# Optimization experiments

Hardware: AMD Instinct MI355X
Metric: run time of the kernel (lower is better)

## Reference

```python
import jax, jax.numpy as jnp
import numpy as np

GAMMA = 1.0
BIG = 1e8  # boundary value used by the original numba kernel


def setup_inputs() -> dict:
    key = jax.random.key(0)
    k1, k2 = jax.random.split(key)
    N, M, d = 4096, 4096, 64
    x = jax.random.normal(k1, (N, d), dtype=jnp.float32)
    y = jax.random.normal(k2, (M, d), dtype=jnp.float32)
    return {"x": x, "y": y}


def _soft_dtw(D, gamma):
    """Soft-DTW DP R[N,M] via anti-diagonal wavefront scan.

    Matches compute_softdtw: R padded with BIG, R[0,0]=0,
    R[i,j] = D[i-1,j-1] + softmin_gamma(R[i-1,j-1], R[i-1,j], R[i,j-1]).
    Diagonals are stored as length-(N+2) vectors indexed by i (j = k - i).
    """
    N, M = D.shape
    ii = jnp.arange(1, N + 1)          # cell row indices 1..N
    inf = jnp.full((N + 2,), BIG, D.dtype)
    r_km2 = inf.at[0].set(0.0)          # diagonal k=0: only R[0,0]=0
    r_km1 = inf                         # diagonal k=1: all boundary

    def step(carry, k):
        r_km2, r_km1 = carry
        j = k - ii                      # column index per row on this diagonal
        valid = (j >= 1) & (j <= M)
        r0 = -r_km2[ii - 1] / gamma     # R[i-1, j-1]
        r1 = -r_km1[ii - 1] / gamma     # R[i-1, j]
        r2 = -r_km1[ii] / gamma         # R[i,   j-1]
        rmax = jnp.maximum(jnp.maximum(r0, r1), r2)
        rsum = jnp.exp(r0 - rmax) + jnp.exp(r1 - rmax) + jnp.exp(r2 - rmax)
        softmin = -gamma * (jnp.log(rsum) + rmax)
        jc = jnp.clip(j - 1, 0, M - 1)
        d_diag = D[ii - 1, jc]          # D[i-1, j-1] along this diagonal
        val = jnp.where(valid, d_diag + softmin, BIG)
        r_k = inf.at[1:N + 1].set(val)
        return (r_km1, r_k), None

    ks = jnp.arange(2, N + M + 1)
    (_, r_last), _ = jax.lax.scan(step, (r_km2, r_km1), ks)
    return r_last[N]                    # R[N, M]


def reference(x, y):
    # squared-euclidean distance matrix: sum((x_i - y_j)^2)
    x2 = jnp.sum(x * x, axis=1)
    y2 = jnp.sum(y * y, axis=1)
    D = x2[:, None] + y2[None, :] - 2.0 * (x @ y.T)  # [N, M]
    N, M = D.shape
    r = _soft_dtw(D, GAMMA)
    return r / (N + M)                   # open_end=False path
```

## Files before the change

### kernel.cpp

```cpp
#include <hip/hip_runtime.h>
#include <hip/hip_fp16.h>

#define Nn 4096
#define Mm 4096
#define NB 64
#define CH 16
#define NCHUNK 260
#define NCHUNKP 262
#define HPITCH 4352
#define HOFF 64
#define LOG2E 1.4426950408889634f
#define LN2 0.6931471805599453f
#define BIGX (1 << 23)

typedef unsigned long long ull;

__device__ __forceinline__ float hw_exp2(float x) { return __builtin_amdgcn_exp2f(x); }
__device__ __forceinline__ float hw_log2(float x) { return __builtin_amdgcn_logf(x); }

__device__ __forceinline__ float dpp_shr1(float v) {
    int r = __builtin_amdgcn_update_dpp(0, __float_as_int(v), 0x138, 0xF, 0xF, false);
    return __int_as_float(r);
}
__device__ __forceinline__ int dpp_shr1_i(int v) {
    return __builtin_amdgcn_update_dpp(0, v, 0x138, 0xF, 0xF, false);
}
__device__ __forceinline__ float dpp_shl1(float v) {
    int r = __builtin_amdgcn_update_dpp(0, __float_as_int(v), 0x130, 0xF, 0xF, false);
    return __int_as_float(r);
}
__device__ __forceinline__ int dpp_shl1_i(int v) {
    return __builtin_amdgcn_update_dpp(0, v, 0x130, 0xF, 0xF, false);
}
__device__ __forceinline__ float half_lo(int w) {
    return __low2float(__builtin_bit_cast(__half2, w));
}
__device__ __forceinline__ float half_hi(int w) {
    return __high2float(__builtin_bit_cast(__half2, w));
}
__device__ __forceinline__ ull packmx(float m, int X) {
    return (ull)__float_as_uint(m) | ((ull)(unsigned)X << 32);
}

__global__ __launch_bounds__(256) void dist_kernel(const float* __restrict__ x,
                                                   const float* __restrict__ y,
                                                   __half* __restrict__ Dsk) {
    __shared__ float xs[64][65];
    __shared__ float ys[80][65];
    __shared__ float dt[64][81];
    __shared__ float x2s[64], y2s[80];
    const int b = blockIdx.y, tj = blockIdx.x, tid = threadIdx.x;

    const float4* x4 = (const float4*)(x + (size_t)b * 64 * 64);
#pragma unroll
    for (int i = 0; i < 4; ++i) {
        int idx = tid + i * 256;
        int r = idx >> 4, c = (idx & 15) * 4;
        float4 v = x4[idx];
        xs[r][c] = v.x; xs[r][c + 1] = v.y; xs[r][c + 2] = v.z; xs[r][c + 3] = v.w;
    }
#pragma unroll
    for (int i = 0; i < 5; ++i) {
        int idx = tid + i * 256;
        int r = idx >> 4, c = (idx & 15) * 4;
        int rowg = tj * 64 + r; if (rowg > Mm - 1) rowg = Mm - 1;
        float4 w = ((const float4*)(y + (size_t)rowg * 64))[c >> 2];
        ys[r][c] = w.x; ys[r][c + 1] = w.y; ys[r][c + 2] = w.z; ys[r][c + 3] = w.w;
    }
    __syncthreads();

    if (tid < 64) {
        float a = 0.f;
#pragma unroll 8
        for (int k = 0; k < 64; ++k) a += xs[tid][k] * xs[tid][k];
        x2s[tid] = a;
    } else if (tid < 144) {
        int r = tid - 64;
        float a = 0.f;
#pragma unroll 8
        for (int k = 0; k < 64; ++k) a += ys[r][k] * ys[r][k];
        y2s[r] = a;
    }
    __syncthreads();

    const int r0 = (tid >> 4) * 4, c0 = (tid & 15) * 5;
    float acc[4][5] = {{0.f}};
#pragma unroll 4
    for (int k = 0; k < 64; ++k) {
        float a0 = xs[r0][k], a1 = xs[r0 + 1][k], a2 = xs[r0 + 2][k], a3 = xs[r0 + 3][k];
#pragma unroll
        for (int j = 0; j < 5; ++j) {
            float bj = ys[c0 + j][k];
            acc[0][j] = fmaf(a0, bj, acc[0][j]);
            acc[1][j] = fmaf(a1, bj, acc[1][j]);
            acc[2][j] = fmaf(a2, bj, acc[2][j]);
            acc[3][j] = fmaf(a3, bj, acc[3][j]);
        }
    }
#pragma unroll
    for (int i = 0; i < 4; ++i)
#pragma unroll
        for (int j = 0; j < 5; ++j)
            dt[r0 + i][c0 + j] =
                (x2s[r0 + i] + y2s[c0 + j] - 2.0f * acc[i][j]) * LOG2E;
    __syncthreads();

    const int l = tid & 63, q = tid >> 6;
    const int ci = ((l + 15) >> 4) + q;
    const int jj0 = 16 * ci - l;
    int w[8];
#pragma unroll
    for (int i = 0; i < 8; ++i) {
        __half2 hh;
        hh.x = __float2half(dt[l][jj0 + 2 * i]);
        hh.y = __float2half(dt[l][jj0 + 2 * i + 1]);
        w[i] = __builtin_bit_cast(int, hh);
    }
    {
        __half* dst = Dsk + (((size_t)b * NCHUNKP + 4 * tj + ci) * 64 + l) * 16;
        int4* d4 = (int4*)dst;
        d4[0] = make_int4(w[0], w[1], w[2], w[3]);
        d4[1] = make_int4(w[4], w[5], w[6], w[7]);
    }
    if (tj == 0 && q == 0) {
        const int cif = l >> 4;
        int wf[8];
#pragma unroll
        for (int i = 0; i < 8; ++i) {
            int ja = 16 * cif - l + 2 * i;     if (ja < 0) ja = 0;
            int jb = 16 * cif - l + 2 * i + 1; if (jb < 0) jb = 0;
            __half2 hh;
            hh.x = __float2half(dt[l][ja]);
            hh.y = __float2half(dt[l][jb]);
            wf[i] = __builtin_bit_cast(int, hh);
        }
        __half* dst = Dsk + (((size_t)b * NCHUNKP + cif) * 64 + l) * 16;
        int4* d4 = (int4*)dst;
        d4[0] = make_int4(wf[0], wf[1], wf[2], wf[3]);
        d4[1] = make_int4(wf[4], wf[5], wf[6], wf[7]);
    }
}

#define PREP(KM, NI, DV) \
    float dv_##KM = (DV); float nf_##KM = __builtin_rintf(dv_##KM); \
    int NI = (int)nf_##KM; float KM = hw_exp2(nf_##KM - dv_##KM);

#define STEP(KM, NI, IDX) do {                                                \
    float shufM = dpp_shr1(lM);                                               \
    int   shufX = dpp_shr1_i(lX);                                             \
    float upM = isL0 ? hRotM : shufM;                                         \
    int   upX = isL0 ? hRotX : shufX;                                         \
    float dgM = isL0 ? hPrevM : psM;                                          \
    int   dgX = isL0 ? hPrevX : psX;                                          \
    hPrevM = hRotM; hPrevX = hRotX;                                           \
    hRotM = dpp_shl1(hRotM); hRotX = dpp_shl1_i(hRotX);                       \
    int Xm = min(min(dgX, upX), lX);                                          \
    float ssum = ldexpf(dgM, Xm - dgX) + ldexpf(upM, Xm - upX) +              \
                 ldexpf(lM, Xm - lX);                                         \
    float mraw = ssum * (KM);                                                 \
    unsigned mb = __float_as_uint(mraw);                                      \
    int e = (int)((mb >> 23) & 0xFFu) - 126;                                  \
    psM = shufM; psX = shufX;                                                 \
    lM = __uint_as_float((mb & 0x807FFFFFu) | 0x3F000000u);                   \
    lX = Xm + (NI) - e;                                                       \
    if (doStore)                                                              \
        __hip_atomic_store(&HoutB[16 * c + (IDX) - 62], packmx(lM, lX),       \
                           __ATOMIC_RELAXED, __HIP_MEMORY_SCOPE_AGENT);       \
} while (0)

__global__ __launch_bounds__(64, 1) void dp_kernel(const __half* __restrict__ Dsk,
                                                   ull* __restrict__ H,
                                                   float* __restrict__ out) {
    const int l = threadIdx.x;
    const int b = blockIdx.x;
    const bool isL0 = (l == 0), isL63 = (l == 63), lastBand = (b == NB - 1);
    const int lt = l & 15;
    const __half* __restrict__ Db = Dsk + ((size_t)b * NCHUNKP * 64 + l) * 16;
    const ull* __restrict__ HinB = H + (size_t)b * HPITCH + HOFF;
    ull* __restrict__ HoutB = H + (size_t)(b + 1) * HPITCH + HOFF;
    const bool doH = (b > 0);
    const bool doStore = (!lastBand) && isL63;

    float lM = 0.5f;  int lX = BIGX;
    float psM = 0.5f; int psX = BIGX;
    float hPrevM = 0.5f; int hPrevX = (b == 0) ? -1 : BIGX;
    float hRotM; int hRotX;
    ull hNextU, hLoadU;
    int4 dn1A, dn1B, dn2A, dn2B;
    float rTM = 0.5f; int rTX = 0;

    {
        const int4* p = (const int4*)Db;
        dn1A = p[0]; dn1B = p[1];
        const int4* q = (const int4*)(Db + 1024);
        dn2A = q[0]; dn2B = q[1];
    }
    if (doH) {
        hNextU = __hip_atomic_load(&HinB[1 + lt],      __ATOMIC_RELAXED, __HIP_MEMORY_SCOPE_AGENT);
        hLoadU = __hip_atomic_load(&HinB[CH + 1 + lt], __ATOMIC_RELAXED, __HIP_MEMORY_SCOPE_AGENT);
    } else {
        hNextU = packmx(0.5f, BIGX);
        hLoadU = packmx(0.5f, BIGX);
    }

    for (int c = 0; c < NCHUNK; ++c) {
        int4 dcA = dn1A, dcB = dn1B;
        dn1A = dn2A; dn1B = dn2B;
        {
            const int4* p = (const int4*)(Db + (size_t)(c + 2) * 1024);
            dn2A = p[0]; dn2B = p[1];
        }
        hRotM = __uint_as_float((unsigned)hNextU);
        hRotX = (int)(unsigned)(hNextU >> 32);
        hNextU = hLoadU;
        if (doH && (c + 2 <= 255))
            hLoadU = __hip_atomic_load(&HinB[16 * (c + 2) + 1 + lt],
                                       __ATOMIC_RELAXED, __HIP_MEMORY_SCOPE_AGENT);
        if (doH && (c <= 255)) {
            while (__ballot(!(hRotM > 0.f))) {
                __builtin_amdgcn_s_sleep(1);
                ull v = __hip_atomic_load(&HinB[16 * c + 1 + lt],
                                          __ATOMIC_RELAXED, __HIP_MEMORY_SCOPE_AGENT);
                hRotM = __uint_as_float((unsigned)v);
                hRotX = (int)(unsigned)(v >> 32);
            }
        }

        PREP(k0,  n0,  half_lo(dcA.x)); PREP(k1,  n1,  half_hi(dcA.x));
        PREP(k2,  n2,  half_lo(dcA.y)); PREP(k3,  n3,  half_hi(dcA.y));
        PREP(k4,  n4,  half_lo(dcA.z)); PREP(k5,  n5,  half_hi(dcA.z));
        PREP(k6,  n6,  half_lo(dcA.w)); PREP(k7,  n7,  half_hi(dcA.w));
        PREP(k8,  n8,  half_lo(dcB.x)); PREP(k9,  n9,  half_hi(dcB.x));
        PREP(k10, n10, half_lo(dcB.y)); PREP(k11, n11, half_hi(dcB.y));
        PREP(k12, n12, half_lo(dcB.z)); PREP(k13, n13, half_hi(dcB.z));
        PREP(k14, n14, half_lo(dcB.w)); PREP(k15, n15, half_hi(dcB.w));

        STEP(k0,  n0,  0);  STEP(k1,  n1,  1);  STEP(k2,  n2,  2);
        STEP(k3,  n3,  3);  STEP(k4,  n4,  4);  STEP(k5,  n5,  5);
        STEP(k6,  n6,  6);  STEP(k7,  n7,  7);  STEP(k8,  n8,  8);
        STEP(k9,  n9,  9);  STEP(k10, n10, 10); STEP(k11, n11, 11);
        STEP(k12, n12, 12); STEP(k13, n13, 13); STEP(k14, n14, 14);
        if (c == NCHUNK - 1) { rTM = lM; rTX = lX; }
        STEP(k15, n15, 15);
    }

    if (lastBand && isL63) {
        float rpr = (float)rTX - hw_log2(rTM);
        out[0] = rpr * (LN2 / (float)(Nn + Mm));
    }
}

extern "C" void kernel_launch(void* const* d_in, const int* in_sizes, int n_in,
                              void* d_out, int out_size, void* d_ws, size_t ws_size,
                              hipStream_t stream) {
    const float* x = (const float*)d_in[0];
    const float* y = (const float*)d_in[1];
    float* out = (float*)d_out;

    char* ws = (char*)d_ws;
    __half* Dsk = (__half*)ws;
    size_t dskBytes = (size_t)NB * NCHUNKP * 64 * 16 * sizeof(__half);
    ull* H = (ull*)(ws + dskBytes);

    dist_kernel<<<dim3(64, 64), 256, 0, stream>>>(x, y, Dsk);
    dp_kernel<<<NB, 64, 0, stream>>>(Dsk, H, out);
}
```

Before: 1.212 ms.

## Group 16 bands per workgroup and pass boundaries through LDS ring buffers

The 64 DP bands now run as 4 workgroups of 16 waves instead of 64 single-wave blocks. Neighbouring bands inside a workgroup hand off boundary values through shared-memory ring buffers with workgroup-scope acquire/release counters. Only bands at workgroup edges still use global atomics. This is meant to cut the latency of cross-band handoff through global memory. The STEP macro is also simplified: a single DPP op with a bound-control old value replaces the lane-0 select logic. The cost is that producers now stall on ring back-pressure, and all 16 waves of a group share one CU.

```diff
diff --git a/kernel.cpp b/kernel.cpp
--- a/kernel.cpp
+++ b/kernel.cpp
@@ -13,18 +13,16 @@
 #define LN2 0.6931471805599453f
 #define BIGX (1 << 23)
 
+#define WAVES 16
+#define NWG 4
+#define RING 512
+#define RINGCH 32
+
 typedef unsigned long long ull;
 
 __device__ __forceinline__ float hw_exp2(float x) { return __builtin_amdgcn_exp2f(x); }
 __device__ __forceinline__ float hw_log2(float x) { return __builtin_amdgcn_logf(x); }
 
-__device__ __forceinline__ float dpp_shr1(float v) {
-    int r = __builtin_amdgcn_update_dpp(0, __float_as_int(v), 0x138, 0xF, 0xF, false);
-    return __int_as_float(r);
-}
-__device__ __forceinline__ int dpp_shr1_i(int v) {
-    return __builtin_amdgcn_update_dpp(0, v, 0x138, 0xF, 0xF, false);
-}
 __device__ __forceinline__ float dpp_shl1(float v) {
     int r = __builtin_amdgcn_update_dpp(0, __float_as_int(v), 0x130, 0xF, 0xF, false);
     return __int_as_float(r);
@@ -146,13 +144,10 @@
     int NI = (int)nf_##KM; float KM = hw_exp2(nf_##KM - dv_##KM);
 
 #define STEP(KM, NI, IDX) do {                                                \
-    float shufM = dpp_shr1(lM);                                               \
-    int   shufX = dpp_shr1_i(lX);                                             \
-    float upM = isL0 ? hRotM : shufM;                                         \
-    int   upX = isL0 ? hRotX : shufX;                                         \
-    float dgM = isL0 ? hPrevM : psM;                                          \
-    int   dgX = isL0 ? hPrevX : psX;                                          \
-    hPrevM = hRotM; hPrevX = hRotX;                                           \
+    float upM = __int_as_float(__builtin_amdgcn_update_dpp(                   \
+        __float_as_int(hRotM), __float_as_int(lM), 0x138, 0xF, 0xF, false));  \
+    int   upX = __builtin_amdgcn_update_dpp(hRotX, lX, 0x138, 0xF, 0xF, false); \
+    float dgM = psM; int dgX = psX;                                           \
     hRotM = dpp_shl1(hRotM); hRotX = dpp_shl1_i(hRotX);                       \
     int Xm = min(min(dgX, upX), lX);                                          \
     float ssum = ldexpf(dgM, Xm - dgX) + ldexpf(upM, Xm - upX) +              \
@@ -160,34 +155,54 @@
     float mraw = ssum * (KM);                                                 \
     unsigned mb = __float_as_uint(mraw);                                      \
     int e = (int)((mb >> 23) & 0xFFu) - 126;                                  \
-    psM = shufM; psX = shufX;                                                 \
+    psM = upM; psX = upX;                                                     \
     lM = __uint_as_float((mb & 0x807FFFFFu) | 0x3F000000u);                   \
     lX = Xm + (NI) - e;                                                       \
-    if (doStore)                                                              \
+    if (doStoreG)                                                             \
         __hip_atomic_store(&HoutB[16 * c + (IDX) - 62], packmx(lM, lX),       \
                            __ATOMIC_RELAXED, __HIP_MEMORY_SCOPE_AGENT);       \
+    else if (doStoreL) {                                                      \
+        int s_ = 16 * c + (IDX) - 62;                                         \
+        if (s_ >= 1) ringW[s_ & (RING - 1)] = packmx(lM, lX);                 \
+    }                                                                         \
 } while (0)
 
-__global__ __launch_bounds__(64, 1) void dp_kernel(const __half* __restrict__ Dsk,
-                                                   ull* __restrict__ H,
-                                                   float* __restrict__ out) {
-    const int l = threadIdx.x;
-    const int b = blockIdx.x;
-    const bool isL0 = (l == 0), isL63 = (l == 63), lastBand = (b == NB - 1);
+__global__ __launch_bounds__(1024, 1) void dp_kernel(const __half* __restrict__ Dsk,
+                                                     ull* __restrict__ H,
+                                                     float* __restrict__ out) {
+    __shared__ ull ring[WAVES - 1][RING];
+    __shared__ int prodCnt[WAVES];
+    __shared__ int consProg[WAVES];
+
+    const int tid = threadIdx.x;
+    const int l = tid & 63, w = tid >> 6, g = blockIdx.x;
+    const int b = (g << 4) | w;
+    const bool isL63 = (l == 63), lastBand = (b == NB - 1);
+    const bool gloCons = (w == 0) && (g > 0);
+    const bool ldsCons = (w > 0);
+    const bool prodG = (w == WAVES - 1) && !lastBand;
+    const bool prodL = (w < WAVES - 1);
+    const bool doStoreG = prodG && isL63;
+    const bool doStoreL = prodL && isL63;
     const int lt = l & 15;
+
+    if (tid < WAVES) { prodCnt[tid] = 0; consProg[tid] = 0; }
+    __syncthreads();
+
     const __half* __restrict__ Db = Dsk + ((size_t)b * NCHUNKP * 64 + l) * 16;
     const ull* __restrict__ HinB = H + (size_t)b * HPITCH + HOFF;
     ull* __restrict__ HoutB = H + (size_t)(b + 1) * HPITCH + HOFF;
-    const bool doH = (b > 0);
-    const bool doStore = (!lastBand) && isL63;
+    ull* __restrict__ ringW = prodL ? &ring[w][0] : &ring[0][0];
+    const ull* __restrict__ ringR = ldsCons ? &ring[w - 1][0] : &ring[0][0];
 
     float lM = 0.5f;  int lX = BIGX;
-    float psM = 0.5f; int psX = BIGX;
-    float hPrevM = 0.5f; int hPrevX = (b == 0) ? -1 : BIGX;
+    float psM = 0.5f;
+    int psX = (b == 0 && l == 0) ? -1 : BIGX;
     float hRotM; int hRotX;
-    ull hNextU, hLoadU;
+    ull hNextU, hLoadU = 0;
     int4 dn1A, dn1B, dn2A, dn2B;
     float rTM = 0.5f; int rTX = 0;
+    int cachedCnt = 0, consSeen = 0;
 
     {
         const int4* p = (const int4*)Db;
@@ -195,12 +210,17 @@
         const int4* q = (const int4*)(Db + 1024);
         dn2A = q[0]; dn2B = q[1];
     }
-    if (doH) {
+    if (gloCons) {
         hNextU = __hip_atomic_load(&HinB[1 + lt],      __ATOMIC_RELAXED, __HIP_MEMORY_SCOPE_AGENT);
         hLoadU = __hip_atomic_load(&HinB[CH + 1 + lt], __ATOMIC_RELAXED, __HIP_MEMORY_SCOPE_AGENT);
+    } else if (ldsCons) {
+        while ((cachedCnt = __hip_atomic_load(&prodCnt[w - 1], __ATOMIC_ACQUIRE,
+                                              __HIP_MEMORY_SCOPE_WORKGROUP)) < 5)
+            __builtin_amdgcn_s_sleep(1);
+        hNextU = ringR[(1 + lt) & (RING - 1)];
     } else {
         hNextU = packmx(0.5f, BIGX);
-        hLoadU = packmx(0.5f, BIGX);
+        hLoadU = hNextU;
     }
 
     for (int c = 0; c < NCHUNK; ++c) {
@@ -212,17 +232,43 @@
         }
         hRotM = __uint_as_float((unsigned)hNextU);
         hRotX = (int)(unsigned)(hNextU >> 32);
-        hNextU = hLoadU;
-        if (doH && (c + 2 <= 255))
-            hLoadU = __hip_atomic_load(&HinB[16 * (c + 2) + 1 + lt],
-                                       __ATOMIC_RELAXED, __HIP_MEMORY_SCOPE_AGENT);
-        if (doH && (c <= 255)) {
-            while (__ballot(!(hRotM > 0.f))) {
+
+        if (gloCons) {
+            hNextU = hLoadU;
+            if (c + 2 <= 255)
+                hLoadU = __hip_atomic_load(&HinB[16 * (c + 2) + 1 + lt],
+                                           __ATOMIC_RELAXED, __HIP_MEMORY_SCOPE_AGENT);
+            if (c <= 255) {
+                while (__ballot(!(hRotM > 0.f))) {
+                    __builtin_amdgcn_s_sleep(1);
+                    ull v = __hip_atomic_load(&HinB[16 * c + 1 + lt],
+                                              __ATOMIC_RELAXED, __HIP_MEMORY_SCOPE_AGENT);
+                    hRotM = __uint_as_float((unsigned)v);
+                    hRotX = (int)(unsigned)(v >> 32);
+                }
+            }
+        } else if (ldsCons) {
+            if (l == 0)
+                __hip_atomic_store(&consProg[w], c, __ATOMIC_RELAXED,
+                                   __HIP_MEMORY_SCOPE_WORKGROUP);
+            if (c + 1 <= 255) {
+                const int need = c + 6;
+                while (cachedCnt < need) {
+                    cachedCnt = __hip_atomic_load(&prodCnt[w - 1], __ATOMIC_ACQUIRE,
+                                                  __HIP_MEMORY_SCOPE_WORKGROUP);
+                    if (cachedCnt >= need) break;
+                    __builtin_amdgcn_s_sleep(1);
+                }
+                hNextU = ringR[(16 * (c + 1) + 1 + lt) & (RING - 1)];
+            }
+        }
+
+        if (prodL && (c - consSeen >= RINGCH - 2)) {
+            while (1) {
+                consSeen = __hip_atomic_load(&consProg[w + 1], __ATOMIC_RELAXED,
+                                             __HIP_MEMORY_SCOPE_WORKGROUP);
+                if (c - consSeen < RINGCH - 2) break;
                 __builtin_amdgcn_s_sleep(1);
-                ull v = __hip_atomic_load(&HinB[16 * c + 1 + lt],
-                                          __ATOMIC_RELAXED, __HIP_MEMORY_SCOPE_AGENT);
-                hRotM = __uint_as_float((unsigned)v);
-                hRotX = (int)(unsigned)(v >> 32);
             }
         }
 
@@ -242,6 +288,10 @@
         STEP(k12, n12, 12); STEP(k13, n13, 13); STEP(k14, n14, 14);
         if (c == NCHUNK - 1) { rTM = lM; rTX = lX; }
         STEP(k15, n15, 15);
+
+        if (doStoreL)
+            __hip_atomic_store(&prodCnt[w], c + 1, __ATOMIC_RELEASE,
+                               __HIP_MEMORY_SCOPE_WORKGROUP);
     }
 
     if (lastBand && isL63) {
@@ -263,5 +313,5 @@
     ull* H = (ull*)(ws + dskBytes);
 
     dist_kernel<<<dim3(64, 64), 256, 0, stream>>>(x, y, Dsk);
-    dp_kernel<<<NB, 64, 0, stream>>>(Dsk, H, out);
-}
+    dp_kernel<<<NWG, WAVES * 64, 0, stream>>>(Dsk, H, out);
+}
```

New measurement: 2.556 ms. 2.11x slower.

## Fold boundary injection into DPP bound_ctrl and add startup cushion wait

Applied to the files above, without the earlier changes.

The step now uses the DPP old-value operand, so lane 0 receives the halo value from hRot directly. This removes the isL0 selects and the hPrev tracking from the inner recurrence, which shortens the serial critical path of each step. Each band also waits at startup until the upstream band is CUSH chunks ahead, and the in-loop spin uses a longer sleep. Together these are meant to reduce contention from polling, at the cost of a longer pipeline fill latency.

```diff
diff --git a/kernel.cpp b/kernel.cpp
--- a/kernel.cpp
+++ b/kernel.cpp
@@ -12,19 +12,13 @@
 #define LOG2E 1.4426950408889634f
 #define LN2 0.6931471805599453f
 #define BIGX (1 << 23)
+#define CUSH 5
 
 typedef unsigned long long ull;
 
 __device__ __forceinline__ float hw_exp2(float x) { return __builtin_amdgcn_exp2f(x); }
 __device__ __forceinline__ float hw_log2(float x) { return __builtin_amdgcn_logf(x); }
 
-__device__ __forceinline__ float dpp_shr1(float v) {
-    int r = __builtin_amdgcn_update_dpp(0, __float_as_int(v), 0x138, 0xF, 0xF, false);
-    return __int_as_float(r);
-}
-__device__ __forceinline__ int dpp_shr1_i(int v) {
-    return __builtin_amdgcn_update_dpp(0, v, 0x138, 0xF, 0xF, false);
-}
 __device__ __forceinline__ float dpp_shl1(float v) {
     int r = __builtin_amdgcn_update_dpp(0, __float_as_int(v), 0x130, 0xF, 0xF, false);
     return __int_as_float(r);
@@ -146,13 +140,10 @@
     int NI = (int)nf_##KM; float KM = hw_exp2(nf_##KM - dv_##KM);
 
 #define STEP(KM, NI, IDX) do {                                                \
-    float shufM = dpp_shr1(lM);                                               \
-    int   shufX = dpp_shr1_i(lX);                                             \
-    float upM = isL0 ? hRotM : shufM;                                         \
-    int   upX = isL0 ? hRotX : shufX;                                         \
-    float dgM = isL0 ? hPrevM : psM;                                          \
-    int   dgX = isL0 ? hPrevX : psX;                                          \
-    hPrevM = hRotM; hPrevX = hRotX;                                           \
+    float upM = __int_as_float(__builtin_amdgcn_update_dpp(                   \
+        __float_as_int(hRotM), __float_as_int(lM), 0x138, 0xF, 0xF, false));  \
+    int   upX = __builtin_amdgcn_update_dpp(hRotX, lX, 0x138, 0xF, 0xF, false); \
+    float dgM = psM; int dgX = psX;                                           \
     hRotM = dpp_shl1(hRotM); hRotX = dpp_shl1_i(hRotX);                       \
     int Xm = min(min(dgX, upX), lX);                                          \
     float ssum = ldexpf(dgM, Xm - dgX) + ldexpf(upM, Xm - upX) +              \
@@ -160,7 +151,7 @@
     float mraw = ssum * (KM);                                                 \
     unsigned mb = __float_as_uint(mraw);                                      \
     int e = (int)((mb >> 23) & 0xFFu) - 126;                                  \
-    psM = shufM; psX = shufX;                                                 \
+    psM = upM; psX = upX;                                                     \
     lM = __uint_as_float((mb & 0x807FFFFFu) | 0x3F000000u);                   \
     lX = Xm + (NI) - e;                                                       \
     if (doStore)                                                              \
@@ -173,7 +164,7 @@
                                                    float* __restrict__ out) {
     const int l = threadIdx.x;
     const int b = blockIdx.x;
-    const bool isL0 = (l == 0), isL63 = (l == 63), lastBand = (b == NB - 1);
+    const bool isL63 = (l == 63), lastBand = (b == NB - 1);
     const int lt = l & 15;
     const __half* __restrict__ Db = Dsk + ((size_t)b * NCHUNKP * 64 + l) * 16;
     const ull* __restrict__ HinB = H + (size_t)b * HPITCH + HOFF;
@@ -182,12 +173,21 @@
     const bool doStore = (!lastBand) && isL63;
 
     float lM = 0.5f;  int lX = BIGX;
-    float psM = 0.5f; int psX = BIGX;
-    float hPrevM = 0.5f; int hPrevX = (b == 0) ? -1 : BIGX;
+    float psM = 0.5f; int psX = (b == 0 && l == 0) ? -1 : BIGX;
     float hRotM; int hRotX;
     ull hNextU, hLoadU;
     int4 dn1A, dn1B, dn2A, dn2B;
     float rTM = 0.5f; int rTX = 0;
+
+    if (doH) {
+        const int gs = 16 * (CUSH - 1) + 1 + lt;
+        while (1) {
+            ull v = __hip_atomic_load(&HinB[gs], __ATOMIC_RELAXED,
+                                      __HIP_MEMORY_SCOPE_AGENT);
+            if (!__ballot(!(__uint_as_float((unsigned)v) > 0.f))) break;
+            __builtin_amdgcn_s_sleep(8);
+        }
+    }
 
     {
         const int4* p = (const int4*)Db;
@@ -218,7 +218,7 @@
                                        __ATOMIC_RELAXED, __HIP_MEMORY_SCOPE_AGENT);
         if (doH && (c <= 255)) {
             while (__ballot(!(hRotM > 0.f))) {
-                __builtin_amdgcn_s_sleep(1);
+                __builtin_amdgcn_s_sleep(16);
                 ull v = __hip_atomic_load(&HinB[16 * c + 1 + lt],
                                           __ATOMIC_RELAXED, __HIP_MEMORY_SCOPE_AGENT);
                 hRotM = __uint_as_float((unsigned)v);
```

After: 1.309 ms. 1.08x slower.
